# Performance work log

Hardware: AMD Instinct MI355X
Metric: run time of the kernel (lower is better)

## Reference

```python
import jax, jax.numpy as jnp
import numpy as np

WS = (2, 6, 12)          # window_size (Z, H, W)
DIM = 192
HEADS = 6
TOW = 240                # type_of_windows = (8//2)*(360//6)
NW = 720                 # total number of windows = 3 * TOW
L = WS[0] * WS[1] * WS[2]  # 144 tokens per window


def _position_index(ws):
    """Replicates EarthAttention3D._construct_index (static int index)."""
    zi = np.arange(ws[0]); zj = -np.arange(ws[0]) * ws[0]
    hi = np.arange(ws[1]); hj = -np.arange(ws[1]) * ws[1]
    w = np.arange(ws[2])
    c1 = np.stack(np.meshgrid(zi, hi, w, indexing='ij')).reshape(3, -1)
    c2 = np.stack(np.meshgrid(zj, hj, w, indexing='ij')).reshape(3, -1)
    coords = (c1[:, :, None] - c2[:, None, :]).transpose(1, 2, 0)  # (L, L, 3)
    coords[:, :, 2] += ws[2] - 1
    coords[:, :, 1] *= 2 * ws[2] - 1
    coords[:, :, 0] *= (2 * ws[2] - 1) * ws[1] * ws[1]
    return coords.sum(-1).reshape(-1)  # (L*L,)

POS_INDEX = jnp.asarray(_position_index(WS))


def setup_inputs() -> dict:
    key = jax.random.key(0)
    ks = jax.random.split(key, 4)
    table_len = (2 * WS[2] - 1) * WS[1] * WS[1] * WS[0] * WS[0]  # 3312
    return {
        "x": jax.random.normal(ks[0], (NW, L, DIM), jnp.float32),
        "mask": jnp.zeros((NW, L, L), jnp.float32),
        "w1": jax.random.normal(ks[1], (3 * DIM, DIM), jnp.float32) * 0.02,
        "b1": jnp.zeros((3 * DIM,), jnp.float32),
        "w2": jax.random.normal(ks[2], (DIM, DIM), jnp.float32) * 0.02,
        "b2": jnp.zeros((DIM,), jnp.float32),
        "bias_table": jax.random.normal(ks[3], (table_len, TOW, HEADS), jnp.float32) * 0.02,
    }


def reference(x, mask, w1, b1, w2, b2, bias_table):
    Wn, Ltok, dim = x.shape
    hd = dim // HEADS
    scale = hd ** -0.5
    # qkv projection: (Wn, L, 3, H, hd) -> q,k,v each (Wn, H, L, hd)
    qkv = (x @ w1.T + b1).reshape(Wn, Ltok, 3, HEADS, hd)
    qkv = jnp.transpose(qkv, (2, 0, 3, 1, 4))
    q, k, v = qkv[0], qkv[1], qkv[2]
    attn = jnp.einsum('whid,whjd->whij', q * scale, k)  # (Wn, H, L, L)
    # Earth-specific bias: gather table -> (L, L, TOW, H) -> (TOW, H, L, L)
    bias = bias_table[POS_INDEX].reshape(Ltok, Ltok, TOW, HEADS)
    bias = jnp.transpose(bias, (2, 3, 0, 1))
    # tile across window axis exactly like the concat loop, then slice
    reps = Wn // TOW + 1
    bias = jnp.tile(bias, (reps, 1, 1, 1))[:Wn][None]  # (1, Wn, H, L, L)
    attn = attn[None] + bias                            # (1, Wn, H, L, L)
    attn = attn + mask[None, :, None, :, :]             # mask.unsqueeze(1).unsqueeze(0)
    attn = jax.nn.softmax(attn, axis=-1)
    out = jnp.einsum('bwhij,whjd->bwhid', attn, v)      # (1, Wn, H, L, hd)
    out = jnp.transpose(out, (0, 1, 3, 2, 4)).reshape(Wn, Ltok, dim)
    out = out @ w2.T + b2
    return out
```

## Files before the change

kernel.cpp:

```cpp
#include <hip/hip_runtime.h>
#include <cstdint>
#include <cstddef>


using short8 = __attribute__((ext_vector_type(8))) short;
using f32x4  = __attribute__((ext_vector_type(4))) float;

constexpr int kNW = 720;
constexpr float kScale = 0.17677669529663687f;
constexpr size_t kQKVElems = (size_t)kNW * 6 * 144 * 32;

__device__ __forceinline__ ushort bf16_rne(float f) {
  uint u = __builtin_bit_cast(uint, f);
  return (ushort)((u + 0x7FFFu + ((u >> 16) & 1u)) >> 16);
}
__device__ __forceinline__ float bf16_to_f(ushort h) {
  uint u = ((uint)h) << 16;
  return __builtin_bit_cast(float, u);
}

__global__ __launch_bounds__(256) void prep_kernel(
    const float* __restrict__ src, ushort* __restrict__ dh,
    ushort* __restrict__ dl, int n)
{
  const int i = blockIdx.x * 256 + threadIdx.x;
  if (i < n) {
    const float f = src[i];
    const ushort h = bf16_rne(f);
    dh[i] = h;
    dl[i] = bf16_rne(f - bf16_to_f(h));
  }
}

__global__ __launch_bounds__(256) void btT_kernel(
    const float* __restrict__ bt, float* __restrict__ btT)
{
  __shared__ float T[48][49];
  const int pb = (blockIdx.x % 69) * 48;
  const int bb = (blockIdx.x / 69) * 48;
  const int tid = threadIdx.x;
  for (int f = tid; f < 2304; f += 256) {
    const int r = f / 48, c = f % 48;
    T[r][c] = bt[(size_t)(pb + r) * 1440 + bb + c];
  }
  __syncthreads();
  for (int f = tid; f < 2304; f += 256) {
    const int r = f % 48, c = f / 48;
    btT[(size_t)(bb + c) * 3312 + pb + r] = T[r][c];
  }
}

template <bool IS_QKV>
__global__ __launch_bounds__(256) void gemm_kernel(
    const float* __restrict__ X, const ushort* __restrict__ Wh,
    const ushort* __restrict__ Wl, const float* __restrict__ bias,
    ushort* __restrict__ o0, ushort* __restrict__ o1, ushort* __restrict__ o2,
    ushort* __restrict__ o3, ushort* __restrict__ o4, ushort* __restrict__ o5,
    float* __restrict__ fout)
{
  __shared__ ushort Ah[64][40], Al[64][40];
  __shared__ ushort Bh[192][40], Bl[192][40];

  const int bid = blockIdx.x;
  const int mtile = IS_QKV ? bid / 3 : bid;
  const int col0  = IS_QKV ? (bid % 3) * 192 : 0;
  const int row0 = mtile * 64;
  const int tid = threadIdx.x;
  const int wv = tid >> 6;
  const int lane = tid & 63;
  const int rr = lane & 15;
  const int kg = lane >> 4;
  const int nbase = wv * 48;

  f32x4 acc[4][3];
#pragma unroll
  for (int a = 0; a < 4; ++a)
#pragma unroll
    for (int b = 0; b < 3; ++b) acc[a][b] = (f32x4){0.f, 0.f, 0.f, 0.f};

  for (int kc = 0; kc < 192; kc += 32) {
#pragma unroll
    for (int u = 0; u < 2; ++u) {
      const int sl = tid * 2 + u;
      const int r = sl >> 3, s = sl & 7;
      float4 xv = *(const float4*)&X[(size_t)(row0 + r) * 192 + kc + s * 4];
      ushort4 hv, lv;
      hv.x = bf16_rne(xv.x); lv.x = bf16_rne(xv.x - bf16_to_f(hv.x));
      hv.y = bf16_rne(xv.y); lv.y = bf16_rne(xv.y - bf16_to_f(hv.y));
      hv.z = bf16_rne(xv.z); lv.z = bf16_rne(xv.z - bf16_to_f(hv.z));
      hv.w = bf16_rne(xv.w); lv.w = bf16_rne(xv.w - bf16_to_f(hv.w));
      *(ushort4*)&Ah[r][s * 4] = hv;
      *(ushort4*)&Al[r][s * 4] = lv;
    }
#pragma unroll
    for (int u = 0; u < 6; ++u) {
      const int sl = tid + u * 256;
      const int n = sl >> 3, s = sl & 7;
      const size_t g = (size_t)(col0 + n) * 192 + kc + s * 4;
      *(uint2*)&Bh[n][s * 4] = *(const uint2*)&Wh[g];
      *(uint2*)&Bl[n][s * 4] = *(const uint2*)&Wl[g];
    }
    __syncthreads();

    short8 ah[4], al_[4], bh[3], bl[3];
#pragma unroll
    for (int mt = 0; mt < 4; ++mt) {
      ah[mt]  = *(const short8*)&Ah[mt * 16 + rr][kg * 8];
      al_[mt] = *(const short8*)&Al[mt * 16 + rr][kg * 8];
    }
#pragma unroll
    for (int nt = 0; nt < 3; ++nt) {
      bh[nt] = *(const short8*)&Bh[nbase + nt * 16 + rr][kg * 8];
      bl[nt] = *(const short8*)&Bl[nbase + nt * 16 + rr][kg * 8];
    }
#pragma unroll
    for (int mt = 0; mt < 4; ++mt)
#pragma unroll
      for (int nt = 0; nt < 3; ++nt) {
        acc[mt][nt] = __builtin_amdgcn_mfma_f32_16x16x32_bf16(ah[mt],  bh[nt], acc[mt][nt], 0, 0, 0);
        acc[mt][nt] = __builtin_amdgcn_mfma_f32_16x16x32_bf16(ah[mt],  bl[nt], acc[mt][nt], 0, 0, 0);
        acc[mt][nt] = __builtin_amdgcn_mfma_f32_16x16x32_bf16(al_[mt], bh[nt], acc[mt][nt], 0, 0, 0);
      }
    __syncthreads();
  }

  if (IS_QKV) {
    const int t = col0 / 192;
    ushort* dh = (t == 0) ? o0 : (t == 1) ? o2 : o4;
    ushort* dl = (t == 0) ? o1 : (t == 1) ? o3 : o5;
    const float sc = (t == 0) ? kScale : 1.0f;
#pragma unroll
    for (int nt = 0; nt < 3; ++nt) {
      const int c0 = nbase + nt * 16;
      const int hh = c0 >> 5;
      const int d0 = (c0 & 31) + rr;
      const float bcol = bias[col0 + c0 + rr];
#pragma unroll
      for (int mt = 0; mt < 4; ++mt)
#pragma unroll
        for (int reg = 0; reg < 4; ++reg) {
          const int grow = row0 + mt * 16 + kg * 4 + reg;
          const int w = grow / 144;
          const int l = grow % 144;
          const float vv = (acc[mt][nt][reg] + bcol) * sc;
          const ushort hv = bf16_rne(vv);
          const size_t idx = (((size_t)(w * 6 + hh)) * 144 + l) * 32 + d0;
          dh[idx] = hv;
          dl[idx] = bf16_rne(vv - bf16_to_f(hv));
        }
    }
  } else {
#pragma unroll
    for (int nt = 0; nt < 3; ++nt) {
      const int c = nbase + nt * 16 + rr;
      const float bcol = bias[c];
#pragma unroll
      for (int mt = 0; mt < 4; ++mt)
#pragma unroll
        for (int reg = 0; reg < 4; ++reg) {
          const int grow = row0 + mt * 16 + kg * 4 + reg;
          fout[(size_t)grow * 192 + c] = acc[mt][nt][reg] + bcol;
        }
    }
  }
}

__global__ __launch_bounds__(576, 5) void attn_kernel(
    const ushort* __restrict__ qh, const ushort* __restrict__ ql,
    const ushort* __restrict__ kh, const ushort* __restrict__ kl,
    const ushort* __restrict__ vh, const ushort* __restrict__ vl,
    const float* __restrict__ mask, const float* __restrict__ btT,
    float* __restrict__ ao)
{
  __shared__ ushort Ks_[2][144][40];
  __shared__ ushort Vt[2][32][168];
  __shared__ float Bs[3312];

  const int bid = blockIdx.x;
  const int wid = (bid & 7) * 540 + (bid >> 3);
  const int w = wid / 6, h = wid % 6;
  const int tid = threadIdx.x;
  const int wave = tid >> 6;
  const int lane = tid & 63;
  const int rr = lane & 15;
  const int kg = lane >> 4;
  const size_t base = (size_t)(w * 6 + h) * 4608;
  const float* mrow = mask + (size_t)w * 20736;
  const float* brow = btT + (size_t)((w % 240) * 6 + h) * 3312;

  for (int f = tid; f < 1152; f += 576) {
    const int l = f >> 3, d0 = (f & 7) * 4;
    *(uint2*)&Ks_[0][l][d0] = *(const uint2*)&kh[base + l * 32 + d0];
    *(uint2*)&Ks_[1][l][d0] = *(const uint2*)&kl[base + l * 32 + d0];
    const ushort4 a = *(const ushort4*)&vh[base + l * 32 + d0];
    Vt[0][d0 + 0][l] = a.x; Vt[0][d0 + 1][l] = a.y;
    Vt[0][d0 + 2][l] = a.z; Vt[0][d0 + 3][l] = a.w;
    const ushort4 b = *(const ushort4*)&vl[base + l * 32 + d0];
    Vt[1][d0 + 0][l] = b.x; Vt[1][d0 + 1][l] = b.y;
    Vt[1][d0 + 2][l] = b.z; Vt[1][d0 + 3][l] = b.w;
  }
  if (tid < 512) {
    const int d = tid >> 4, j = 144 + (tid & 15);
    Vt[0][d][j] = 0;
    Vt[1][d][j] = 0;
  }
  for (int p = tid; p < 3312; p += 576) Bs[p] = brow[p];
  __syncthreads();

  const int i0 = wave * 16;
  const int i = i0 + rr;
  const short8 qbh = *(const short8*)&qh[base + (size_t)i * 32 + kg * 8];
  const short8 qbl = *(const short8*)&ql[base + (size_t)i * 32 + kg * 8];
  const int pi = 828 * (i / 72) + 23 * ((i / 12) % 6) + (i % 12) + 11;

  f32x4 acc[9];
#pragma unroll
  for (int jt = 0; jt < 9; ++jt) {
    const short8 kah = *(const short8*)&Ks_[0][jt * 16 + rr][kg * 8];
    const short8 kal = *(const short8*)&Ks_[1][jt * 16 + rr][kg * 8];
    f32x4 c = (f32x4){0.f, 0.f, 0.f, 0.f};
    c = __builtin_amdgcn_mfma_f32_16x16x32_bf16(kah, qbh, c, 0, 0, 0);
    c = __builtin_amdgcn_mfma_f32_16x16x32_bf16(kah, qbl, c, 0, 0, 0);
    c = __builtin_amdgcn_mfma_f32_16x16x32_bf16(kal, qbh, c, 0, 0, 0);
    const int jb = jt * 16 + kg * 4;
    const int pjb = 1656 * (jb / 72) + 138 * ((jb / 12) % 6) - (jb % 12);
    const float4 mv = *(const float4*)&mrow[(size_t)i * 144 + jb];
    const int bb = pi + pjb;
    c[0] += Bs[bb]     + mv.x;
    c[1] += Bs[bb - 1] + mv.y;
    c[2] += Bs[bb - 2] + mv.z;
    c[3] += Bs[bb - 3] + mv.w;
    acc[jt] = c;
  }

  float m = -1e30f;
#pragma unroll
  for (int jt = 0; jt < 9; ++jt)
    m = fmaxf(m, fmaxf(fmaxf(acc[jt][0], acc[jt][1]),
                       fmaxf(acc[jt][2], acc[jt][3])));
  m = fmaxf(m, __shfl_xor(m, 16));
  m = fmaxf(m, __shfl_xor(m, 32));
  float s = 0.f;
#pragma unroll
  for (int jt = 0; jt < 9; ++jt)
#pragma unroll
    for (int r = 0; r < 4; ++r) {
      acc[jt][r] = __expf(acc[jt][r] - m);
      s += acc[jt][r];
    }
  s += __shfl_xor(s, 16);
  s += __shfl_xor(s, 32);
  const float inv = 1.0f / s;

  uint wh_[10][2], wl_[10][2];
#pragma unroll
  for (int jt = 0; jt < 9; ++jt)
#pragma unroll
    for (int u = 0; u < 2; ++u) {
      const float p0 = acc[jt][2 * u] * inv, p1 = acc[jt][2 * u + 1] * inv;
      const ushort h0 = bf16_rne(p0), h1 = bf16_rne(p1);
      const ushort l0 = bf16_rne(p0 - bf16_to_f(h0));
      const ushort l1 = bf16_rne(p1 - bf16_to_f(h1));
      wh_[jt][u] = (uint)h0 | ((uint)h1 << 16);
      wl_[jt][u] = (uint)l0 | ((uint)l1 << 16);
    }
  wh_[9][0] = 0; wh_[9][1] = 0; wl_[9][0] = 0; wl_[9][1] = 0;

  __syncthreads();

  uint* scrw = (uint*)((ushort*)&Ks_[0][0][0] + wave * 1280);
  f32x4 oacc[2] = {(f32x4){0.f, 0.f, 0.f, 0.f}, (f32x4){0.f, 0.f, 0.f, 0.f}};
#pragma unroll
  for (int ks = 0; ks < 5; ++ks) {
    const int jtA = 2 * ks, jtB = 2 * ks + 1;
    *(uint2*)&scrw[rr * 20 + 2 * kg]           = make_uint2(wh_[jtA][0], wh_[jtA][1]);
    *(uint2*)&scrw[rr * 20 + 8 + 2 * kg]       = make_uint2(wh_[jtB][0], wh_[jtB][1]);
    *(uint2*)&scrw[320 + rr * 20 + 2 * kg]     = make_uint2(wl_[jtA][0], wl_[jtA][1]);
    *(uint2*)&scrw[320 + rr * 20 + 8 + 2 * kg] = make_uint2(wl_[jtB][0], wl_[jtB][1]);
    asm volatile("s_waitcnt lgkmcnt(0)" ::: "memory");
    const ushort* scr = (const ushort*)scrw;
    const short8 pfh = *(const short8*)&scr[rr * 40 + kg * 8];
    const short8 pfl = *(const short8*)&scr[640 + rr * 40 + kg * 8];
#pragma unroll
    for (int dt = 0; dt < 2; ++dt) {
      const short8 vfh = *(const short8*)&Vt[0][dt * 16 + rr][ks * 32 + kg * 8];
      const short8 vfl = *(const short8*)&Vt[1][dt * 16 + rr][ks * 32 + kg * 8];
      oacc[dt] = __builtin_amdgcn_mfma_f32_16x16x32_bf16(pfh, vfh, oacc[dt], 0, 0, 0);
      oacc[dt] = __builtin_amdgcn_mfma_f32_16x16x32_bf16(pfh, vfl, oacc[dt], 0, 0, 0);
      oacc[dt] = __builtin_amdgcn_mfma_f32_16x16x32_bf16(pfl, vfh, oacc[dt], 0, 0, 0);
    }
  }

#pragma unroll
  for (int dt = 0; dt < 2; ++dt)
#pragma unroll
    for (int r = 0; r < 4; ++r)
      ao[(size_t)(w * 144 + i0 + kg * 4 + r) * 192 + h * 32 + dt * 16 + rr] =
          oacc[dt][r];
}

extern "C" void kernel_launch(void* const* d_in, const int* in_sizes, int n_in,
                              void* d_out, int out_size, void* d_ws, size_t ws_size,
                              hipStream_t stream)
{
  const float* x    = (const float*)d_in[0];
  const float* mask = (const float*)d_in[1];
  const float* w1   = (const float*)d_in[2];
  const float* b1   = (const float*)d_in[3];
  const float* w2   = (const float*)d_in[4];
  const float* b2   = (const float*)d_in[5];
  const float* bt   = (const float*)d_in[6];
  float* out = (float*)d_out;

  ushort* qh = (ushort*)d_ws;
  ushort* ql = qh + kQKVElems;
  ushort* kh = ql + kQKVElems;
  ushort* kl = kh + kQKVElems;
  ushort* vh = kl + kQKVElems;
  ushort* vl = vh + kQKVElems;
  float*  ao = (float*)(vl + kQKVElems);
  ushort* w1h = (ushort*)ao;
  ushort* w1l = w1h + 110592;
  ushort* w2h = qh;
  ushort* w2l = w2h + 36864;
  float* btT = out;

  btT_kernel<<<69 * 30, 256, 0, stream>>>(bt, btT);
  prep_kernel<<<432, 256, 0, stream>>>(w1, w1h, w1l, 110592);
  gemm_kernel<true><<<1620 * 3, 256, 0, stream>>>(
      x, w1h, w1l, b1, qh, ql, kh, kl, vh, vl, nullptr);
  attn_kernel<<<4320, 576, 0, stream>>>(qh, ql, kh, kl, vh, vl, mask, btT, ao);
  prep_kernel<<<144, 256, 0, stream>>>(w2, w2h, w2l, 36864);
  gemm_kernel<false><<<1620, 256, 0, stream>>>(
      ao, w2h, w2l, b2, nullptr, nullptr, nullptr, nullptr, nullptr, nullptr, out);
}
```

Before: 406.7 us.

## Pack hi/lo bf16 pairs, enlarge GEMM tiles, load bias directly to registers

Q/K/V and the attention output are now stored as packed 32-bit hi/lo bf16 pairs, so each element is written and read with one access instead of two. The attention output becomes a pre-split pair, so the output GEMM no longer does the fp32-to-bf16 split. The GEMM moves to 128-row tiles with 512 threads, halving redundant weight tile loads per row. In attention, the shared-memory bias table staging is replaced by per-thread prefetched float4 bias and mask loads issued before the K/V staging. The trade-off is higher register pressure and unaligned float4 bias reads from global memory.

```diff
diff --git a/kernel.cpp b/kernel.cpp
--- a/kernel.cpp
+++ b/kernel.cpp
@@ -17,6 +17,11 @@
 __device__ __forceinline__ float bf16_to_f(ushort h) {
   uint u = ((uint)h) << 16;
   return __builtin_bit_cast(float, u);
+}
+__device__ __forceinline__ uint pack_hl(float f) {
+  const ushort h = bf16_rne(f);
+  const ushort l = bf16_rne(f - bf16_to_f(h));
+  return ((uint)h << 16) | l;
 }
 
 __global__ __launch_bounds__(256) void prep_kernel(
@@ -51,26 +56,24 @@
 }
 
 template <bool IS_QKV>
-__global__ __launch_bounds__(256) void gemm_kernel(
-    const float* __restrict__ X, const ushort* __restrict__ Wh,
-    const ushort* __restrict__ Wl, const float* __restrict__ bias,
-    ushort* __restrict__ o0, ushort* __restrict__ o1, ushort* __restrict__ o2,
-    ushort* __restrict__ o3, ushort* __restrict__ o4, ushort* __restrict__ o5,
+__global__ __launch_bounds__(512, 6) void gemm_kernel(
+    const float* __restrict__ Xf, const uint* __restrict__ Xp,
+    const ushort* __restrict__ Wh, const ushort* __restrict__ Wl,
+    const float* __restrict__ bias,
+    uint* __restrict__ qp, uint* __restrict__ kp, uint* __restrict__ vp,
     float* __restrict__ fout)
 {
-  __shared__ ushort Ah[64][40], Al[64][40];
+  __shared__ ushort Ah[128][40], Al[128][40];
   __shared__ ushort Bh[192][40], Bl[192][40];
 
   const int bid = blockIdx.x;
   const int mtile = IS_QKV ? bid / 3 : bid;
   const int col0  = IS_QKV ? (bid % 3) * 192 : 0;
-  const int row0 = mtile * 64;
+  const int row0 = mtile * 128;
   const int tid = threadIdx.x;
-  const int wv = tid >> 6;
-  const int lane = tid & 63;
-  const int rr = lane & 15;
-  const int kg = lane >> 4;
-  const int nbase = wv * 48;
+  const int wave = tid >> 6, lane = tid & 63;
+  const int rr = lane & 15, kg = lane >> 4;
+  const int wm = wave >> 2, wn = wave & 3;
 
   f32x4 acc[4][3];
 #pragma unroll
@@ -81,37 +84,50 @@
   for (int kc = 0; kc < 192; kc += 32) {
 #pragma unroll
     for (int u = 0; u < 2; ++u) {
-      const int sl = tid * 2 + u;
+      const int sl = tid + u * 512;
       const int r = sl >> 3, s = sl & 7;
-      float4 xv = *(const float4*)&X[(size_t)(row0 + r) * 192 + kc + s * 4];
-      ushort4 hv, lv;
-      hv.x = bf16_rne(xv.x); lv.x = bf16_rne(xv.x - bf16_to_f(hv.x));
-      hv.y = bf16_rne(xv.y); lv.y = bf16_rne(xv.y - bf16_to_f(hv.y));
-      hv.z = bf16_rne(xv.z); lv.z = bf16_rne(xv.z - bf16_to_f(hv.z));
-      hv.w = bf16_rne(xv.w); lv.w = bf16_rne(xv.w - bf16_to_f(hv.w));
-      *(ushort4*)&Ah[r][s * 4] = hv;
-      *(ushort4*)&Al[r][s * 4] = lv;
-    }
-#pragma unroll
-    for (int u = 0; u < 6; ++u) {
-      const int sl = tid + u * 256;
-      const int n = sl >> 3, s = sl & 7;
-      const size_t g = (size_t)(col0 + n) * 192 + kc + s * 4;
-      *(uint2*)&Bh[n][s * 4] = *(const uint2*)&Wh[g];
-      *(uint2*)&Bl[n][s * 4] = *(const uint2*)&Wl[g];
+      if constexpr (IS_QKV) {
+        float4 xv = *(const float4*)&Xf[(size_t)(row0 + r) * 192 + kc + s * 4];
+        ushort4 hv, lv;
+        hv.x = bf16_rne(xv.x); lv.x = bf16_rne(xv.x - bf16_to_f(hv.x));
+        hv.y = bf16_rne(xv.y); lv.y = bf16_rne(xv.y - bf16_to_f(hv.y));
+        hv.z = bf16_rne(xv.z); lv.z = bf16_rne(xv.z - bf16_to_f(hv.z));
+        hv.w = bf16_rne(xv.w); lv.w = bf16_rne(xv.w - bf16_to_f(hv.w));
+        *(ushort4*)&Ah[r][s * 4] = hv;
+        *(ushort4*)&Al[r][s * 4] = lv;
+      } else {
+        uint4 a = *(const uint4*)&Xp[(size_t)(row0 + r) * 192 + kc + s * 4];
+        uint2 hh, ll;
+        hh.x = (a.x >> 16) | (a.y & 0xffff0000u);
+        hh.y = (a.z >> 16) | (a.w & 0xffff0000u);
+        ll.x = (a.x & 0xffffu) | (a.y << 16);
+        ll.y = (a.z & 0xffffu) | (a.w << 16);
+        *(uint2*)&Ah[r][s * 4] = hh;
+        *(uint2*)&Al[r][s * 4] = ll;
+      }
+    }
+#pragma unroll
+    for (int u = 0; u < 3; ++u) {
+      const int idx = tid + u * 512;
+      const int n = idx >> 3, s2 = idx & 7;
+      const size_t g = (size_t)(col0 + n) * 192 + kc + s2 * 4;
+      *(uint2*)&Bh[n][s2 * 4] = *(const uint2*)&Wh[g];
+      *(uint2*)&Bl[n][s2 * 4] = *(const uint2*)&Wl[g];
     }
     __syncthreads();
 
     short8 ah[4], al_[4], bh[3], bl[3];
 #pragma unroll
     for (int mt = 0; mt < 4; ++mt) {
-      ah[mt]  = *(const short8*)&Ah[mt * 16 + rr][kg * 8];
-      al_[mt] = *(const short8*)&Al[mt * 16 + rr][kg * 8];
+      const int r = wm * 64 + mt * 16 + rr;
+      ah[mt]  = *(const short8*)&Ah[r][kg * 8];
+      al_[mt] = *(const short8*)&Al[r][kg * 8];
     }
 #pragma unroll
     for (int nt = 0; nt < 3; ++nt) {
-      bh[nt] = *(const short8*)&Bh[nbase + nt * 16 + rr][kg * 8];
-      bl[nt] = *(const short8*)&Bl[nbase + nt * 16 + rr][kg * 8];
+      const int n = wn * 48 + nt * 16 + rr;
+      bh[nt] = *(const short8*)&Bh[n][kg * 8];
+      bl[nt] = *(const short8*)&Bl[n][kg * 8];
     }
 #pragma unroll
     for (int mt = 0; mt < 4; ++mt)
@@ -126,12 +142,11 @@
 
   if (IS_QKV) {
     const int t = col0 / 192;
-    ushort* dh = (t == 0) ? o0 : (t == 1) ? o2 : o4;
-    ushort* dl = (t == 0) ? o1 : (t == 1) ? o3 : o5;
+    uint* dst = (t == 0) ? qp : (t == 1) ? kp : vp;
     const float sc = (t == 0) ? kScale : 1.0f;
 #pragma unroll
     for (int nt = 0; nt < 3; ++nt) {
-      const int c0 = nbase + nt * 16;
+      const int c0 = wn * 48 + nt * 16;
       const int hh = c0 >> 5;
       const int d0 = (c0 & 31) + rr;
       const float bcol = bias[col0 + c0 + rr];
@@ -139,79 +154,94 @@
       for (int mt = 0; mt < 4; ++mt)
 #pragma unroll
         for (int reg = 0; reg < 4; ++reg) {
-          const int grow = row0 + mt * 16 + kg * 4 + reg;
+          const int grow = row0 + wm * 64 + mt * 16 + kg * 4 + reg;
           const int w = grow / 144;
           const int l = grow % 144;
-          const float vv = (acc[mt][nt][reg] + bcol) * sc;
-          const ushort hv = bf16_rne(vv);
-          const size_t idx = (((size_t)(w * 6 + hh)) * 144 + l) * 32 + d0;
-          dh[idx] = hv;
-          dl[idx] = bf16_rne(vv - bf16_to_f(hv));
+          dst[(((size_t)(w * 6 + hh)) * 144 + l) * 32 + d0] =
+              pack_hl((acc[mt][nt][reg] + bcol) * sc);
         }
     }
   } else {
 #pragma unroll
     for (int nt = 0; nt < 3; ++nt) {
-      const int c = nbase + nt * 16 + rr;
+      const int c = wn * 48 + nt * 16 + rr;
       const float bcol = bias[c];
 #pragma unroll
       for (int mt = 0; mt < 4; ++mt)
 #pragma unroll
         for (int reg = 0; reg < 4; ++reg) {
-          const int grow = row0 + mt * 16 + kg * 4 + reg;
+          const int grow = row0 + wm * 64 + mt * 16 + kg * 4 + reg;
           fout[(size_t)grow * 192 + c] = acc[mt][nt][reg] + bcol;
         }
     }
   }
 }
 
-__global__ __launch_bounds__(576, 5) void attn_kernel(
-    const ushort* __restrict__ qh, const ushort* __restrict__ ql,
-    const ushort* __restrict__ kh, const ushort* __restrict__ kl,
-    const ushort* __restrict__ vh, const ushort* __restrict__ vl,
-    const float* __restrict__ mask, const float* __restrict__ btT,
-    float* __restrict__ ao)
+__global__ __launch_bounds__(576, 6) void attn_kernel(
+    const uint* __restrict__ qp, const uint* __restrict__ kp,
+    const uint* __restrict__ vp, const float* __restrict__ mask,
+    const float* __restrict__ btT, uint* __restrict__ aop)
 {
   __shared__ ushort Ks_[2][144][40];
   __shared__ ushort Vt[2][32][168];
-  __shared__ float Bs[3312];
 
   const int bid = blockIdx.x;
   const int wid = (bid & 7) * 540 + (bid >> 3);
   const int w = wid / 6, h = wid % 6;
   const int tid = threadIdx.x;
-  const int wave = tid >> 6;
-  const int lane = tid & 63;
-  const int rr = lane & 15;
-  const int kg = lane >> 4;
+  const int wave = tid >> 6, lane = tid & 63;
+  const int rr = lane & 15, kg = lane >> 4;
   const size_t base = (size_t)(w * 6 + h) * 4608;
   const float* mrow = mask + (size_t)w * 20736;
   const float* brow = btT + (size_t)((w % 240) * 6 + h) * 3312;
 
+  const int i0 = wave * 16;
+  const int i = i0 + rr;
+  const int pi = 828 * (i / 72) + 23 * ((i / 12) % 6) + (i % 12) + 11;
+
+  const uint4 qa = *(const uint4*)&qp[base + (size_t)i * 32 + kg * 8];
+  const uint4 qb = *(const uint4*)&qp[base + (size_t)i * 32 + kg * 8 + 4];
+  float4 mv[9], bv[9];
+#pragma unroll
+  for (int jt = 0; jt < 9; ++jt) {
+    const int jb = jt * 16 + kg * 4;
+    mv[jt] = *(const float4*)&mrow[(size_t)i * 144 + jb];
+    const int pjb = 1656 * (jb / 72) + 138 * ((jb / 12) % 6) - (jb % 12);
+    bv[jt] = *(const float4*)&brow[pi + pjb - 3];
+  }
+
   for (int f = tid; f < 1152; f += 576) {
     const int l = f >> 3, d0 = (f & 7) * 4;
-    *(uint2*)&Ks_[0][l][d0] = *(const uint2*)&kh[base + l * 32 + d0];
-    *(uint2*)&Ks_[1][l][d0] = *(const uint2*)&kl[base + l * 32 + d0];
-    const ushort4 a = *(const ushort4*)&vh[base + l * 32 + d0];
-    Vt[0][d0 + 0][l] = a.x; Vt[0][d0 + 1][l] = a.y;
-    Vt[0][d0 + 2][l] = a.z; Vt[0][d0 + 3][l] = a.w;
-    const ushort4 b = *(const ushort4*)&vl[base + l * 32 + d0];
-    Vt[1][d0 + 0][l] = b.x; Vt[1][d0 + 1][l] = b.y;
-    Vt[1][d0 + 2][l] = b.z; Vt[1][d0 + 3][l] = b.w;
+    const uint4 kv = *(const uint4*)&kp[base + l * 32 + d0];
+    ushort4 hk, lk;
+    hk.x = (ushort)(kv.x >> 16); lk.x = (ushort)(kv.x & 0xffff);
+    hk.y = (ushort)(kv.y >> 16); lk.y = (ushort)(kv.y & 0xffff);
+    hk.z = (ushort)(kv.z >> 16); lk.z = (ushort)(kv.z & 0xffff);
+    hk.w = (ushort)(kv.w >> 16); lk.w = (ushort)(kv.w & 0xffff);
+    *(ushort4*)&Ks_[0][l][d0] = hk;
+    *(ushort4*)&Ks_[1][l][d0] = lk;
+    const uint4 vv = *(const uint4*)&vp[base + l * 32 + d0];
+    Vt[0][d0 + 0][l] = (ushort)(vv.x >> 16); Vt[1][d0 + 0][l] = (ushort)(vv.x & 0xffff);
+    Vt[0][d0 + 1][l] = (ushort)(vv.y >> 16); Vt[1][d0 + 1][l] = (ushort)(vv.y & 0xffff);
+    Vt[0][d0 + 2][l] = (ushort)(vv.z >> 16); Vt[1][d0 + 2][l] = (ushort)(vv.z & 0xffff);
+    Vt[0][d0 + 3][l] = (ushort)(vv.w >> 16); Vt[1][d0 + 3][l] = (ushort)(vv.w & 0xffff);
   }
   if (tid < 512) {
     const int d = tid >> 4, j = 144 + (tid & 15);
     Vt[0][d][j] = 0;
     Vt[1][d][j] = 0;
   }
-  for (int p = tid; p < 3312; p += 576) Bs[p] = brow[p];
   __syncthreads();
 
-  const int i0 = wave * 16;
-  const int i = i0 + rr;
-  const short8 qbh = *(const short8*)&qh[base + (size_t)i * 32 + kg * 8];
-  const short8 qbl = *(const short8*)&ql[base + (size_t)i * 32 + kg * 8];
-  const int pi = 828 * (i / 72) + 23 * ((i / 12) % 6) + (i % 12) + 11;
+  union { short8 v; uint u[4]; } QH, QL;
+  QH.u[0] = (qa.x >> 16) | (qa.y & 0xffff0000u);
+  QH.u[1] = (qa.z >> 16) | (qa.w & 0xffff0000u);
+  QH.u[2] = (qb.x >> 16) | (qb.y & 0xffff0000u);
+  QH.u[3] = (qb.z >> 16) | (qb.w & 0xffff0000u);
+  QL.u[0] = (qa.x & 0xffffu) | (qa.y << 16);
+  QL.u[1] = (qa.z & 0xffffu) | (qa.w << 16);
+  QL.u[2] = (qb.x & 0xffffu) | (qb.y << 16);
+  QL.u[3] = (qb.z & 0xffffu) | (qb.w << 16);
 
   f32x4 acc[9];
 #pragma unroll
@@ -219,17 +249,13 @@
     const short8 kah = *(const short8*)&Ks_[0][jt * 16 + rr][kg * 8];
     const short8 kal = *(const short8*)&Ks_[1][jt * 16 + rr][kg * 8];
     f32x4 c = (f32x4){0.f, 0.f, 0.f, 0.f};
-    c = __builtin_amdgcn_mfma_f32_16x16x32_bf16(kah, qbh, c, 0, 0, 0);
-    c = __builtin_amdgcn_mfma_f32_16x16x32_bf16(kah, qbl, c, 0, 0, 0);
-    c = __builtin_amdgcn_mfma_f32_16x16x32_bf16(kal, qbh, c, 0, 0, 0);
-    const int jb = jt * 16 + kg * 4;
-    const int pjb = 1656 * (jb / 72) + 138 * ((jb / 12) % 6) - (jb % 12);
-    const float4 mv = *(const float4*)&mrow[(size_t)i * 144 + jb];
-    const int bb = pi + pjb;
-    c[0] += Bs[bb]     + mv.x;
-    c[1] += Bs[bb - 1] + mv.y;
-    c[2] += Bs[bb - 2] + mv.z;
-    c[3] += Bs[bb - 3] + mv.w;
+    c = __builtin_amdgcn_mfma_f32_16x16x32_bf16(kah, QH.v, c, 0, 0, 0);
+    c = __builtin_amdgcn_mfma_f32_16x16x32_bf16(kah, QL.v, c, 0, 0, 0);
+    c = __builtin_amdgcn_mfma_f32_16x16x32_bf16(kal, QH.v, c, 0, 0, 0);
+    c[0] += bv[jt].w + mv[jt].x;
+    c[1] += bv[jt].z + mv[jt].y;
+    c[2] += bv[jt].y + mv[jt].z;
+    c[3] += bv[jt].x + mv[jt].w;
     acc[jt] = c;
   }
 
@@ -295,8 +321,8 @@
   for (int dt = 0; dt < 2; ++dt)
 #pragma unroll
     for (int r = 0; r < 4; ++r)
-      ao[(size_t)(w * 144 + i0 + kg * 4 + r) * 192 + h * 32 + dt * 16 + rr] =
-          oacc[dt][r];
+      aop[(size_t)(w * 144 + i0 + kg * 4 + r) * 192 + h * 32 + dt * 16 + rr] =
+          pack_hl(oacc[dt][r]);
 }
 
 extern "C" void kernel_launch(void* const* d_in, const int* in_sizes, int n_in,
@@ -312,25 +338,22 @@
   const float* bt   = (const float*)d_in[6];
   float* out = (float*)d_out;
 
-  ushort* qh = (ushort*)d_ws;
-  ushort* ql = qh + kQKVElems;
-  ushort* kh = ql + kQKVElems;
-  ushort* kl = kh + kQKVElems;
-  ushort* vh = kl + kQKVElems;
-  ushort* vl = vh + kQKVElems;
-  float*  ao = (float*)(vl + kQKVElems);
-  ushort* w1h = (ushort*)ao;
+  uint* qp  = (uint*)d_ws;
+  uint* kp  = qp + kQKVElems;
+  uint* vp  = kp + kQKVElems;
+  uint* aop = vp + kQKVElems;
+  ushort* w1h = (ushort*)aop;
   ushort* w1l = w1h + 110592;
-  ushort* w2h = qh;
+  ushort* w2h = (ushort*)qp;
   ushort* w2l = w2h + 36864;
   float* btT = out;
 
   btT_kernel<<<69 * 30, 256, 0, stream>>>(bt, btT);
   prep_kernel<<<432, 256, 0, stream>>>(w1, w1h, w1l, 110592);
-  gemm_kernel<true><<<1620 * 3, 256, 0, stream>>>(
-      x, w1h, w1l, b1, qh, ql, kh, kl, vh, vl, nullptr);
-  attn_kernel<<<4320, 576, 0, stream>>>(qh, ql, kh, kl, vh, vl, mask, btT, ao);
+  gemm_kernel<true><<<810 * 3, 512, 0, stream>>>(
+      x, nullptr, w1h, w1l, b1, qp, kp, vp, nullptr);
+  attn_kernel<<<4320, 576, 0, stream>>>(qp, kp, vp, mask, btT, aop);
   prep_kernel<<<144, 256, 0, stream>>>(w2, w2h, w2l, 36864);
-  gemm_kernel<false><<<1620, 256, 0, stream>>>(
-      ao, w2h, w2l, b2, nullptr, nullptr, nullptr, nullptr, nullptr, nullptr, out);
-}
+  gemm_kernel<false><<<810, 512, 0, stream>>>(
+      nullptr, aop, w2h, w2l, b2, nullptr, nullptr, nullptr, out);
+}
```

After: 651.3 us. 60.1% more time.
